# Optimization experiments

Hardware: AMD Instinct MI355X
Metric: run time of the kernel (lower is better)

The kernel has to match this reference:

```python
import jax, jax.numpy as jnp
import numpy as np
import math

B = 2; SEQ = 4096; D_MODEL = 768; D_STATE = 128; D_CONV = 4; EXPAND = 2; HEAD_DIM = 64
D_INNER = EXPAND * D_MODEL; D_SSM = D_INNER; NH = D_SSM // HEAD_DIM  # 24 heads
CONV_DIM = D_SSM + 2 * D_STATE; CHUNK = 256
D_IN_PROJ = 2 * D_INNER + 2 * D_STATE + NH


def causal_conv1d(x, w, b):
    # x: [B, C, L]; w: [C, W] depthwise kernel; left-pad for causality; silu activation
    W = w.shape[-1]; L = x.shape[-1]
    xp = jnp.pad(x, ((0, 0), (0, 0), (W - 1, 0)))
    y = b[None, :, None] + sum(xp[:, :, k:k + L] * w[None, :, k, None] for k in range(W))
    return jax.nn.silu(y)


def segsum(a):
    # a: [..., S] -> [..., S, S]; entry (i,j) = sum_{k=j+1..i} a_k for i>=j, -inf above diag
    S = a.shape[-1]
    cs = jnp.cumsum(a, -1)
    d = cs[..., :, None] - cs[..., None, :]
    mask = jnp.tril(jnp.ones((S, S), bool))
    return jnp.where(mask, d, -jnp.inf)


def ssd_chunk_scan(x, dt, A, Bm, Cm, Dp, chunk):
    # Mamba2 SSD chunked selective scan. x:[b,l,h,p] dt:[b,l,h] A:[h] Bm,Cm:[b,l,n] Dp:[h]
    b, l, h, p = x.shape; n = Bm.shape[-1]; nc = l // chunk
    xc = x.reshape(b, nc, chunk, h, p)
    Bc = Bm.reshape(b, nc, chunk, n)
    Cc = Cm.reshape(b, nc, chunk, n)
    dtc = dt.reshape(b, nc, chunk, h)
    a = jnp.transpose(A[None, None, None, :] * dtc, (0, 3, 1, 2))  # [b,h,c,s]
    Acs = jnp.cumsum(a, -1)
    Lm = jnp.exp(segsum(a))  # [b,h,c,s,s] lower-triangular decay
    # intra-chunk (diagonal block) outputs
    Ydiag = jnp.einsum('bcsn,bczn,bhcsz,bczh,bczhp->bcshp', Cc, Bc, Lm, dtc, xc)
    # per-chunk end states
    decay_states = jnp.exp(Acs[..., -1:] - Acs)  # [b,h,c,s]
    states = jnp.einsum('bczn,bhcz,bczh,bczhp->bchpn', Bc, decay_states, dtc, xc)
    # inter-chunk recurrence over nc chunks (small) via scan
    decay_chunk = jnp.exp(Acs[..., -1])  # [b,h,c]
    def step(hcar, inp):
        dcy, st = inp
        return dcy[..., None, None] * hcar + st, hcar  # emit state entering chunk
    _, prev = jax.lax.scan(step, jnp.zeros_like(states[:, 0]),
                           (jnp.moveaxis(decay_chunk, -1, 0), jnp.moveaxis(states, 1, 0)))
    prev = jnp.moveaxis(prev, 0, 1)  # [b,c,h,p,n]
    Yoff = jnp.einsum('bcsn,bchpn,bhcs->bcshp', Cc, prev, jnp.exp(Acs))
    return (Ydiag + Yoff).reshape(b, l, h, p) + Dp[None, None, :, None] * x


def _forward(u, time_diff, W_in, b_in, conv_w, conv_b, tconv1_w, tconv1_b,
             tconv2_w, tconv2_b, mlp_w1, mlp_b1, mlp_w2, mlp_b2, gate_w, gate_b,
             ln_w, ln_b, A_log, dt_bias, Dp, norm_w, W_out, b_out):
    silu = jax.nn.silu
    zxbcdt = u @ W_in.T + b_in  # [B,L,d_in_proj], d_mlp=0
    z = zxbcdt[..., :D_SSM]
    xBC = zxbcdt[..., D_SSM:D_SSM + CONV_DIM]
    dt = zxbcdt[..., D_SSM + CONV_DIM:]  # [B,L,H]
    A = -jnp.exp(A_log)
    xBC = jnp.transpose(causal_conv1d(jnp.transpose(xBC, (0, 2, 1)), conv_w, conv_b), (0, 2, 1))
    # time-gated dt path (time_diff: [B,H,L])
    ts = silu(time_diff @ mlp_w1.T + mlp_b1) @ mlp_w2.T + mlp_b2
    tdt = ts * time_diff
    tdt = causal_conv1d(tdt, tconv1_w, tconv1_b)
    tdt = causal_conv1d(tdt, tconv2_w, tconv2_b)  # [B,H,L]
    final_dt = dt * jnp.transpose(tdt, (0, 2, 1))
    x = xBC[..., :D_SSM]
    Bm = xBC[..., D_SSM:D_SSM + D_STATE]
    Cm = xBC[..., D_SSM + D_STATE:]
    dt_sp = jax.nn.softplus(final_dt + dt_bias)
    xh = x.reshape(x.shape[0], x.shape[1], NH, HEAD_DIM)
    y = ssd_chunk_scan(xh, dt_sp, A, Bm, Cm, Dp, CHUNK).reshape(x.shape[0], x.shape[1], D_SSM)
    # gated RMSNorm (norm_before_gate=False): gate first, then normalize
    yg = y * silu(z)
    y = yg * jax.lax.rsqrt(jnp.mean(yg * yg, -1, keepdims=True) + 1e-12) * norm_w
    out = y @ W_out.T + b_out
    # time residual gate + LayerNorm over seq_len
    tg = jax.nn.sigmoid(time_diff @ gate_w.T + gate_b)  # [B,H,1]
    tmix = tg * time_diff + (1.0 - tg) * tdt
    mu = jnp.mean(tmix, -1, keepdims=True)
    var = jnp.mean((tmix - mu) ** 2, -1, keepdims=True)
    time_out = (tmix - mu) * jax.lax.rsqrt(var + 1e-12) * ln_w + ln_b
    return out, time_out


def setup_inputs():
    key = jax.random.key(0)
    ks = jax.random.split(key, 16)
    def nrm(k, shape, scale=0.02):
        return jax.random.normal(k, shape, jnp.float32) * scale
    dtv = jnp.exp(jax.random.uniform(ks[10], (NH,), jnp.float32) * (math.log(0.1) - math.log(0.001)) + math.log(0.001))
    dtv = jnp.clip(dtv, 1e-4)
    dt_bias = dtv + jnp.log(-jnp.expm1(-dtv))
    A_log = jnp.log(jax.random.uniform(ks[11], (NH,), jnp.float32, 1.0, 16.0))
    return dict(
        u=jax.random.normal(ks[0], (B, SEQ, D_MODEL), jnp.float32),
        time_diff=jax.random.uniform(ks[1], (B, NH, SEQ), jnp.float32),
        W_in=nrm(ks[2], (D_IN_PROJ, D_MODEL)), b_in=jnp.zeros((D_IN_PROJ,), jnp.float32),
        conv_w=nrm(ks[3], (CONV_DIM, D_CONV), 0.2), conv_b=jnp.zeros((CONV_DIM,), jnp.float32),
        tconv1_w=nrm(ks[4], (NH, D_CONV), 0.2), tconv1_b=jnp.zeros((NH,), jnp.float32),
        tconv2_w=nrm(ks[5], (NH, D_CONV), 0.2), tconv2_b=jnp.zeros((NH,), jnp.float32),
        mlp_w1=nrm(ks[6], (SEQ, SEQ)), mlp_b1=jnp.zeros((SEQ,), jnp.float32),
        mlp_w2=nrm(ks[7], (SEQ, SEQ)), mlp_b2=jnp.zeros((SEQ,), jnp.float32),
        gate_w=nrm(ks[8], (1, SEQ)), gate_b=jnp.zeros((1,), jnp.float32),
        ln_w=jnp.ones((SEQ,), jnp.float32), ln_b=jnp.zeros((SEQ,), jnp.float32),
        A_log=A_log, dt_bias=dt_bias, Dp=jnp.ones((NH,), jnp.float32),
        norm_w=jnp.ones((D_SSM,), jnp.float32),
        W_out=nrm(ks[9], (D_MODEL, D_INNER)), b_out=jnp.zeros((D_MODEL,), jnp.float32),
    )


def reference(u, time_diff, W_in, b_in, conv_w, conv_b, tconv1_w, tconv1_b,
              tconv2_w, tconv2_b, mlp_w1, mlp_b1, mlp_w2, mlp_b2, gate_w, gate_b,
              ln_w, ln_b, A_log, dt_bias, Dp, norm_w, W_out, b_out):
    return _forward(u, time_diff, W_in, b_in, conv_w, conv_b, tconv1_w, tconv1_b,
                    tconv2_w, tconv2_b, mlp_w1, mlp_b1, mlp_w2, mlp_b2, gate_w, gate_b,
                    ln_w, ln_b, A_log, dt_bias, Dp, norm_w, W_out, b_out)
```

## Files before the change

### kernel.cpp

```cpp
#include <hip/hip_runtime.h>
#include <math.h>

#define BB 2
#define SEQ 4096
#define DMODEL 768
#define DSTATE 128
#define NHH 24
#define HDIM 64
#define DSSM 1536
#define CDIM 1792
#define CHK 256
#define NC 16
#define DPROJ 3352
#define MR (BB*SEQ)
#define KSPLIT 32
#define XSTR 1920
#define CT 16
#define SXS 270
#define STS 134

typedef __attribute__((ext_vector_type(8))) short bf16x8;
typedef __attribute__((ext_vector_type(8))) unsigned short u16x8;
typedef __attribute__((ext_vector_type(4))) float f32x4;

__device__ __forceinline__ float siluf(float x) { return x / (1.0f + expf(-x)); }

__device__ __forceinline__ unsigned short f2bf(float f) {
    unsigned u = __float_as_uint(f);
    unsigned r = (u + 0x7fffu + ((u >> 16) & 1u)) >> 16;
    return (unsigned short)r;
}

__device__ __forceinline__ float bf2f(unsigned short u) {
    return __uint_as_float(((unsigned)u) << 16);
}

__device__ __forceinline__ float4 bf2f4(ushort4 v) {
    float4 o;
    o.x = bf2f(v.x); o.y = bf2f(v.y); o.z = bf2f(v.z); o.w = bf2f(v.w);
    return o;
}

__device__ __forceinline__ void gload_lds16(const void* g, void* l) {
    __builtin_amdgcn_global_load_lds((const __attribute__((address_space(1))) unsigned int*)g,
                                     (__attribute__((address_space(3))) unsigned int*)l, 16, 0, 0);
}

__global__ __launch_bounds__(256) void cvt_bf16_k(const float* __restrict__ in,
    unsigned short* __restrict__ out, int n_valid, int n_total)
{
    int i = (blockIdx.x * 256 + threadIdx.x) * 4;
    if (i >= n_total) return;
    ushort4 o;
    if (i + 3 < n_valid) {
        float4 v = *(const float4*)&in[i];
        o.x = f2bf(v.x); o.y = f2bf(v.y); o.z = f2bf(v.z); o.w = f2bf(v.w);
    } else {
        o.x = (i + 0 < n_valid) ? f2bf(in[i + 0]) : 0;
        o.y = (i + 1 < n_valid) ? f2bf(in[i + 1]) : 0;
        o.z = (i + 2 < n_valid) ? f2bf(in[i + 2]) : 0;
        o.w = (i + 3 < n_valid) ? f2bf(in[i + 3]) : 0;
    }
    *(ushort4*)&out[i] = o;
}

__global__ __launch_bounds__(256) void gemm_mfma_dual(
    const unsigned short* __restrict__ A,
    const unsigned short* __restrict__ B1, const float* __restrict__ bias1,
    unsigned short* __restrict__ C1, int N1, int NT1, int nbias1, int NWG1,
    const unsigned short* __restrict__ B2, const float* __restrict__ bias2,
    unsigned short* __restrict__ C2, int N2, int NT2, int nbias2,
    int K, int KT)
{
    __shared__ unsigned short SMEM[24576];
    const int tid = threadIdx.x;
    const int w = tid >> 6, l = tid & 63;
    const int wr = w >> 1, wc = w & 1;
    const int lr = l & 15, lk = l >> 4;
    int nwg = gridDim.x, bid = blockIdx.x;
    int wg = (nwg & 7) ? bid : ((bid & 7) * (nwg >> 3) + (bid >> 3));
    const unsigned short* B;
    const float* bias;
    unsigned short* C;
    int N, NT, nbias;
    if (wg < NWG1) { B = B1; bias = bias1; C = C1; N = N1; NT = NT1; nbias = nbias1; }
    else { wg -= NWG1; B = B2; bias = bias2; C = C2; N = N2; NT = NT2; nbias = nbias2; }
    const int m0 = (wg / NT) * 128, n0 = (wg % NT) * 128;
    f32x4 acc[4][4] = {};
    const int i16 = w * 64 + l;
    const int row0 = i16 >> 2, sl = i16 & 3;
    const size_t ga0 = (size_t)(m0 + row0) * K + sl * 8;
    const size_t ga1 = (size_t)(m0 + row0 + 64) * K + sl * 8;
    const size_t gb0 = (size_t)(n0 + row0) * K + sl * 8;
    const size_t gb1 = (size_t)(n0 + row0 + 64) * K + sl * 8;
    const int lo0 = (w * 64) * 8;
    const int lo1 = (256 + w * 64) * 8;

#define STAGE(bb, kt) { int ko = (kt) * 32; int bs = (bb) * 8192;            \
      gload_lds16(A + ga0 + ko, &SMEM[bs + lo0]);                            \
      gload_lds16(A + ga1 + ko, &SMEM[bs + lo1]);                            \
      gload_lds16(B + gb0 + ko, &SMEM[bs + 4096 + lo0]);                     \
      gload_lds16(B + gb1 + ko, &SMEM[bs + 4096 + lo1]); }

    STAGE(0, 0);
    STAGE(1, 1);
    for (int kt = 0; kt < KT; ++kt) {
        if (kt + 1 < KT) {
            asm volatile("s_waitcnt vmcnt(4)" ::: "memory");
        } else {
            asm volatile("s_waitcnt vmcnt(0)" ::: "memory");
        }
        __builtin_amdgcn_s_barrier();
        if (kt + 2 < KT) STAGE((kt + 2) % 3, kt + 2);
        int bs = (kt % 3) * 8192;
        bf16x8 af[4], bg[4];
#pragma unroll
        for (int mi = 0; mi < 4; ++mi)
            af[mi] = *(const bf16x8*)&SMEM[bs + (wr * 64 + mi * 16 + lr) * 32 + lk * 8];
#pragma unroll
        for (int nj = 0; nj < 4; ++nj)
            bg[nj] = *(const bf16x8*)&SMEM[bs + 4096 + (wc * 64 + nj * 16 + lr) * 32 + lk * 8];
#pragma unroll
        for (int mi = 0; mi < 4; ++mi)
#pragma unroll
            for (int nj = 0; nj < 4; ++nj)
                acc[mi][nj] = __builtin_amdgcn_mfma_f32_16x16x32_bf16(af[mi], bg[nj], acc[mi][nj], 0, 0, 0);
    }
#undef STAGE
    {
        unsigned short* CL = SMEM;
#pragma unroll
        for (int half = 0; half < 2; ++half) {
            __syncthreads();
            if (wr == half) {
#pragma unroll
                for (int nj = 0; nj < 4; ++nj) {
                    int col = n0 + wc * 64 + nj * 16 + lr;
                    float bz = (col < nbias) ? bias[col] : 0.f;
                    int cl = wc * 64 + nj * 16 + lr;
#pragma unroll
                    for (int mi = 0; mi < 4; ++mi)
#pragma unroll
                        for (int r = 0; r < 4; ++r)
                            CL[(mi * 16 + lk * 4 + r) * 136 + cl] = f2bf(acc[mi][nj][r] + bz);
                }
            }
            __syncthreads();
            for (int i = tid; i < 1024; i += 256) {
                int rr = i >> 4, c8 = (i & 15) * 8;
                int m = m0 + half * 64 + rr;
                *(u16x8*)&C[(size_t)m * N + n0 + c8] = *(const u16x8*)&CL[rr * 136 + c8];
            }
        }
    }
}

__global__ __launch_bounds__(256) void gemm_skinny_nt(const float* __restrict__ A,
    const float* __restrict__ Bw, float* __restrict__ part, int N, int K)
{
    __shared__ float sA[48 * 33];
    __shared__ float sB[128 * 33];
    const int nb = blockIdx.x, kb = blockIdx.y;
    const int n0 = nb * 128;
    const int KS = K / KSPLIT;
    const int k0 = kb * KS;
    const int tid = threadIdx.x;
    const int tx = tid & 31, ty = tid >> 5;
    float acc[6][4] = {{0.f}};
    for (int kc = 0; kc < KS; kc += 32) {
        if (kc) __syncthreads();
        for (int i = tid; i < 384; i += 256) {
            int m = i >> 3, k4 = (i & 7) * 4;
            float4 v = *(const float4*)&A[(size_t)m * K + k0 + kc + k4];
            sA[m * 33 + k4 + 0] = v.x; sA[m * 33 + k4 + 1] = v.y;
            sA[m * 33 + k4 + 2] = v.z; sA[m * 33 + k4 + 3] = v.w;
        }
        for (int i = tid; i < 1024; i += 256) {
            int n = i >> 3, k4 = (i & 7) * 4;
            float4 v = *(const float4*)&Bw[(size_t)(n0 + n) * K + k0 + kc + k4];
            sB[n * 33 + k4 + 0] = v.x; sB[n * 33 + k4 + 1] = v.y;
            sB[n * 33 + k4 + 2] = v.z; sB[n * 33 + k4 + 3] = v.w;
        }
        __syncthreads();
#pragma unroll 8
        for (int kk = 0; kk < 32; ++kk) {
            float a[6], b[4];
#pragma unroll
            for (int r = 0; r < 6; ++r) a[r] = sA[(ty * 6 + r) * 33 + kk];
#pragma unroll
            for (int j = 0; j < 4; ++j) b[j] = sB[(tx + j * 32) * 33 + kk];
#pragma unroll
            for (int r = 0; r < 6; ++r)
#pragma unroll
                for (int j = 0; j < 4; ++j)
                    acc[r][j] = fmaf(a[r], b[j], acc[r][j]);
        }
    }
    float* pb = part + (size_t)kb * 48 * N;
#pragma unroll
    for (int r = 0; r < 6; ++r)
#pragma unroll
        for (int j = 0; j < 4; ++j)
            pb[(size_t)(ty * 6 + r) * N + n0 + tx + j * 32] = acc[r][j];
}

__global__ __launch_bounds__(256) void conv_skinny_k(const unsigned short* __restrict__ xbc,
    const float* __restrict__ cw, const float* __restrict__ cb,
    unsigned short* __restrict__ out,
    const float* __restrict__ skA, const float* __restrict__ skB,
    float* __restrict__ skPart, int skN, int skK, int NWGC)
{
    __shared__ __align__(16) unsigned char SMEMRAW[23232];
    int bid = blockIdx.x;
    int tid = threadIdx.x;
    if (bid >= NWGC) {
        float* sA = (float*)SMEMRAW;
        float* sB = (float*)(SMEMRAW + 48 * 33 * 4);
        int t = bid - NWGC;
        int nb = t & 31, kb = t >> 5;
        const int n0 = nb * 128;
        const int KS = skK / KSPLIT;
        const int k0 = kb * KS;
        const int tx = tid & 31, ty = tid >> 5;
        float acc[6][4] = {{0.f}};
        for (int kc = 0; kc < KS; kc += 32) {
            if (kc) __syncthreads();
            for (int i = tid; i < 384; i += 256) {
                int m = i >> 3, k4 = (i & 7) * 4;
                float4 v = *(const float4*)&skA[(size_t)m * skK + k0 + kc + k4];
                sA[m * 33 + k4 + 0] = v.x; sA[m * 33 + k4 + 1] = v.y;
                sA[m * 33 + k4 + 2] = v.z; sA[m * 33 + k4 + 3] = v.w;
            }
            for (int i = tid; i < 1024; i += 256) {
                int n = i >> 3, k4 = (i & 7) * 4;
                float4 v = *(const float4*)&skB[(size_t)(n0 + n) * skK + k0 + kc + k4];
                sB[n * 33 + k4 + 0] = v.x; sB[n * 33 + k4 + 1] = v.y;
                sB[n * 33 + k4 + 2] = v.z; sB[n * 33 + k4 + 3] = v.w;
            }
            __syncthreads();
#pragma unroll 8
            for (int kk = 0; kk < 32; ++kk) {
                float a[6], b[4];
#pragma unroll
                for (int r = 0; r < 6; ++r) a[r] = sA[(ty * 6 + r) * 33 + kk];
#pragma unroll
                for (int j = 0; j < 4; ++j) b[j] = sB[(tx + j * 32) * 33 + kk];
#pragma unroll
                for (int r = 0; r < 6; ++r)
#pragma unroll
                    for (int j = 0; j < 4; ++j)
                        acc[r][j] = fmaf(a[r], b[j], acc[r][j]);
            }
        }
        float* pb = skPart + (size_t)kb * 48 * skN;
#pragma unroll
        for (int r = 0; r < 6; ++r)
#pragma unroll
            for (int j = 0; j < 4; ++j)
                pb[(size_t)(ty * 6 + r) * skN + n0 + tx + j * 32] = acc[r][j];
        return;
    }
    int idx = bid * 256 + tid;
    int slot = idx % 448;
    int g = idx / 448;
    int c4 = slot * 4;
    int b = g / (SEQ / CT);
    int t0 = (g % (SEQ / CT)) * CT;
    size_t rb = (size_t)b * SEQ;
    float4 cw0 = *(const float4*)&cw[(c4 + 0) * 4];
    float4 cw1 = *(const float4*)&cw[(c4 + 1) * 4];
    float4 cw2 = *(const float4*)&cw[(c4 + 2) * 4];
    float4 cw3 = *(const float4*)&cw[(c4 + 3) * 4];
    float4 cbv = *(const float4*)&cb[c4];
    float4 zero = {0.f, 0.f, 0.f, 0.f};
    float4 w0, w1, w2;
    w0 = (t0 - 3 >= 0) ? bf2f4(*(const ushort4*)&xbc[(rb + t0 - 3) * XSTR + c4]) : zero;
    w1 = (t0 - 2 >= 0) ? bf2f4(*(const ushort4*)&xbc[(rb + t0 - 2) * XSTR + c4]) : zero;
    w2 = (t0 - 1 >= 0) ? bf2f4(*(const ushort4*)&xbc[(rb + t0 - 1) * XSTR + c4]) : zero;
#pragma unroll
    for (int i = 0; i < CT; ++i) {
        int t = t0 + i;
        float4 w3 = bf2f4(*(const ushort4*)&xbc[(rb + t) * XSTR + c4]);
        float a0 = cbv.x + w0.x * cw0.x + w1.x * cw0.y + w2.x * cw0.z + w3.x * cw0.w;
        float a1 = cbv.y + w0.y * cw1.x + w1.y * cw1.y + w2.y * cw1.z + w3.y * cw1.w;
        float a2 = cbv.z + w0.z * cw2.x + w1.z * cw2.y + w2.z * cw2.z + w3.z * cw2.w;
        float a3 = cbv.w + w0.w * cw3.x + w1.w * cw3.y + w2.w * cw3.z + w3.w * cw3.w;
        ushort4 o;
        o.x = f2bf(siluf(a0)); o.y = f2bf(siluf(a1));
        o.z = f2bf(siluf(a2)); o.w = f2bf(siluf(a3));
        *(ushort4*)&out[(rb + t) * CDIM + c4] = o;
        w0 = w1; w1 = w2; w2 = w3;
    }
}

__global__ __launch_bounds__(256) void reduce_part_k(const float* __restrict__ part,
    const float* __restrict__ bias, float* __restrict__ out, int N, int act)
{
    int idx = blockIdx.x * 256 + threadIdx.x;
    if (idx >= 48 * N) return;
    int n = idx % N;
    float s = bias[n];
#pragma unroll
    for (int kb = 0; kb < KSPLIT; ++kb) s += part[(size_t)kb * 48 * N + idx];
    if (act) s = siluf(s);
    out[idx] = s;
}

__global__ __launch_bounds__(256) void time_conv_k(const float* __restrict__ ts,
    const float* __restrict__ td, const float* __restrict__ w1, const float* __restrict__ b1,
    const float* __restrict__ w2, const float* __restrict__ b2, float* __restrict__ tdt)
{
    __shared__ float u0[SEQ];
    __shared__ float u1[SEQ];
    int row = blockIdx.x, h = row % NHH;
    const float* tsr = ts + (size_t)row * SEQ;
    const float* tdr = td + (size_t)row * SEQ;
    for (int i = threadIdx.x; i < SEQ; i += 256) u0[i] = tsr[i] * tdr[i];
    __syncthreads();
    float wa[4], wb[4];
#pragma unroll
    for (int k = 0; k < 4; ++k) { wa[k] = w1[h * 4 + k]; wb[k] = w2[h * 4 + k]; }
    float ba = b1[h], bbv = b2[h];
    for (int i = threadIdx.x; i < SEQ; i += 256) {
        float acc = ba;
#pragma unroll
        for (int k = 0; k < 4; ++k) { int tt = i + k - 3; if (tt >= 0) acc = fmaf(u0[tt], wa[k], acc); }
        u1[i] = siluf(acc);
    }
    __syncthreads();
    for (int i = threadIdx.x; i < SEQ; i += 256) {
        float acc = bbv;
#pragma unroll
        for (int k = 0; k < 4; ++k) { int tt = i + k - 3; if (tt >= 0) acc = fmaf(u1[tt], wb[k], acc); }
        tdt[(size_t)row * SEQ + i] = siluf(acc);
    }
}

__global__ __launch_bounds__(256) void dtsp_cum_k(const unsigned short* __restrict__ r1,
    const float* __restrict__ tdt, const float* __restrict__ dt_bias,
    const float* __restrict__ A_log, float* __restrict__ dtp, float* __restrict__ acs)
{
    __shared__ float wsum[4];
    int blk = blockIdx.x;
    int c = blk % NC;
    int bh = blk / NC;
    int h = bh % NHH, b = bh / NHH;
    int tid = threadIdx.x;
    int s = c * CHK + tid;
    size_t base = (size_t)bh * SEQ + s;
    float x = bf2f(r1[((size_t)(b * SEQ + s)) * XSTR + CDIM + h]) * tdt[base] + dt_bias[h];
    float dt = (x > 20.0f) ? x : log1pf(expf(x));
    dtp[base] = dt;
    float Ah = -expf(A_log[h]);
    float v = Ah * dt;
    int ln = tid & 63;
#pragma unroll
    for (int off = 1; off < 64; off <<= 1) {
        float t = __shfl_up(v, off, 64);
        if (ln >= off) v += t;
    }
    if (ln == 63) wsum[tid >> 6] = v;
    __syncthreads();
    float add = 0.f;
    int wv = tid >> 6;
#pragma unroll
    for (int i = 0; i < 3; ++i)
        if (i < wv) add += wsum[i];
    acs[base] = v + add;
}

__global__ __launch_bounds__(256) void ssd_states_sraw_k(const unsigned short* __restrict__ xc,
    const float* __restrict__ dtp, const float* __restrict__ acs_g,
    float* __restrict__ st, unsigned short* __restrict__ sraw)
{
    __shared__ float s_coef[256];
    __shared__ unsigned short SXT[64 * STS];
    __shared__ unsigned short SBT[128 * STS];
    int bid = blockIdx.x;
    int blk = (gridDim.x & 7) ? bid : ((bid & 7) * (gridDim.x >> 3) + (bid >> 3));
    int tid = threadIdx.x;
    int w = tid >> 6, l = tid & 63;
    int lr = l & 15, lk = l >> 4;
    if (blk >= BB * NC * NHH) {
        int t = blk - BB * NC * NHH;
        int bc = t / 10, tile = t % 10;
        int rem = tile, st_i = 0;
        for (st_i = 0; ; ++st_i) { if (rem < st_i + 1) break; rem -= st_i + 1; }
        int zt = rem;
        int b = bc / NC, c = bc % NC;
        size_t rowbase = (size_t)b * SEQ + c * CHK;
        for (int i = tid; i < 64 * 32; i += 256) {
            int r = i >> 5, c4 = (i & 31) * 4;
            *(ushort4*)&SXT[r * STS + c4] = *(const ushort4*)&xc[(rowbase + st_i * 64 + r) * CDIM + DSSM + DSTATE + c4];
            *(ushort4*)&SBT[r * STS + c4] = *(const ushort4*)&xc[(rowbase + zt * 64 + r) * CDIM + DSSM + c4];
        }
        __syncthreads();
        f32x4 d[4] = {};
#pragma unroll
        for (int kt = 0; kt < 4; ++kt) {
            bf16x8 av = *(const bf16x8*)&SXT[(w * 16 + lr) * STS + kt * 32 + lk * 8];
            bf16x8 bv[4];
#pragma unroll
            for (int nj = 0; nj < 4; ++nj)
                bv[nj] = *(const bf16x8*)&SBT[(nj * 16 + lr) * STS + kt * 32 + lk * 8];
#pragma unroll
            for (int nj = 0; nj < 4; ++nj)
                d[nj] = __builtin_amdgcn_mfma_f32_16x16x32_bf16(av, bv[nj], d[nj], 0, 0, 0);
        }
        unsigned short* tp = sraw + (size_t)bc * 16 * 4096 + (size_t)(st_i * 4 + zt) * 4096;
#pragma unroll
        for (int nj = 0; nj < 4; ++nj)
#pragma unroll
            for (int r = 0; r < 4; ++r)
                tp[(w * 16 + lk * 4 + r) * 64 + nj * 16 + lr] = f2bf(d[nj][r]);
        return;
    }
    int h = blk % NHH, c = (blk / NHH) % NC, b = blk / (NHH * NC);
    size_t rowbase = (size_t)b * SEQ + c * CHK;
    size_t dbase = (size_t)(b * NHH + h) * SEQ + c * CHK;
    float alv = acs_g[dbase + 255];
    s_coef[tid] = expf(alv - acs_g[dbase + tid]) * dtp[dbase + tid];
    __syncthreads();
    f32x4 acc[4][2] = {};
    for (int z0 = 0; z0 < CHK; z0 += 128) {
        if (z0) __syncthreads();
        for (int i = tid; i < 128 * 8; i += 256) {
            int zz = i >> 3, p8 = (i & 7) * 8;
            float sc = s_coef[z0 + zz];
            u16x8 v = *(const u16x8*)&xc[(rowbase + z0 + zz) * CDIM + h * HDIM + p8];
#pragma unroll
            for (int e = 0; e < 8; ++e)
                SXT[(p8 + e) * STS + zz] = f2bf(bf2f(v[e]) * sc);
        }
        for (int i = tid; i < 128 * 16; i += 256) {
            int zz = i >> 4, n8 = (i & 15) * 8;
            u16x8 v = *(const u16x8*)&xc[(rowbase + z0 + zz) * CDIM + DSSM + n8];
#pragma unroll
            for (int e = 0; e < 8; ++e)
                SBT[(n8 + e) * STS + zz] = v[e];
        }
        __syncthreads();
#pragma unroll
        for (int kt = 0; kt < 4; ++kt) {
            bf16x8 av[4], bv[2];
#pragma unroll
            for (int mi = 0; mi < 4; ++mi)
                av[mi] = *(const bf16x8*)&SXT[(mi * 16 + lr) * STS + kt * 32 + lk * 8];
#pragma unroll
            for (int nj = 0; nj < 2; ++nj)
                bv[nj] = *(const bf16x8*)&SBT[(w * 32 + nj * 16 + lr) * STS + kt * 32 + lk * 8];
#pragma unroll
            for (int mi = 0; mi < 4; ++mi)
#pragma unroll
                for (int nj = 0; nj < 2; ++nj)
                    acc[mi][nj] = __builtin_amdgcn_mfma_f32_16x16x32_bf16(av[mi], bv[nj], acc[mi][nj], 0, 0, 0);
        }
    }
    size_t base = (size_t)blk * (HDIM * DSTATE);
#pragma unroll
    for (int mi = 0; mi < 4; ++mi)
#pragma unroll
        for (int r = 0; r < 4; ++r) {
            int p = mi * 16 + lk * 4 + r;
#pragma unroll
            for (int nj = 0; nj < 2; ++nj)
                st[base + p * DSTATE + w * 32 + nj * 16 + lr] = acc[mi][nj][r];
        }
}

__global__ __launch_bounds__(256) void ssd_scan_k(const float* __restrict__ st,
    const float* __restrict__ acs_g, unsigned short* __restrict__ pv16)
{
    int b = blockIdx.x / NHH, h = blockIdx.x % NHH;
    int tid = threadIdx.x;
    float carry[32];
#pragma unroll
    for (int j = 0; j < 32; ++j) carry[j] = 0.f;
    for (int c = 0; c < NC; ++c) {
        int bch = (b * NC + c) * NHH + h;
        size_t base = (size_t)bch * (HDIM * DSTATE);
        float dcy = expf(acs_g[(size_t)(b * NHH + h) * SEQ + c * CHK + 255]);
#pragma unroll
        for (int j = 0; j < 32; ++j) {
            pv16[base + tid + j * 256] = f2bf(carry[j]);
            carry[j] = fmaf(dcy, carry[j], st[base + tid + j * 256]);
        }
    }
}

__global__ __launch_bounds__(256) void ssd_y2_k(const unsigned short* __restrict__ xc,
    const float* __restrict__ dtp, const float* __restrict__ acs_g,
    const unsigned short* __restrict__ sraw, const unsigned short* __restrict__ pv16,
    const float* __restrict__ Dp, unsigned short* __restrict__ Ybf)
{
    __shared__ unsigned short SXT[32 * SXS];
    int bid = blockIdx.x;
    int blk2 = (gridDim.x & 7) ? bid : ((bid & 7) * (gridDim.x >> 3) + (bid >> 3));
    int half = blk2 & 1;
    int blk = blk2 >> 1;
    int h = blk % NHH;
    int c = (blk / NHH) % NC;
    int b = blk / (NHH * NC);
    int tid = threadIdx.x;
    int w = tid >> 6, l = tid & 63;
    int lr = l & 15, lk = l >> 4;
    int pbase = half * 32;
    size_t rowbase = (size_t)b * SEQ + c * CHK;
    size_t dbase = (size_t)(b * NHH + h) * SEQ + c * CHK;
    for (int i = tid; i < 256 * 4; i += 256) {
        int z = i >> 2, p8 = (i & 3) * 8;
        float az0q = acs_g[dbase + (z & 192)];
        float e = az0q - acs_g[dbase + z];
        if (e > 60.f) e = 60.f;
        float sc = expf(e) * dtp[dbase + z];
        u16x8 v = *(const u16x8*)&xc[(rowbase + z) * CDIM + h * HDIM + pbase + p8];
#pragma unroll
        for (int e2 = 0; e2 < 8; ++e2)
            SXT[(p8 + e2) * SXS + z] = f2bf(bf2f(v[e2]) * sc);
    }
    float az0w = acs_g[dbase + w * 64];
    float esw[4][4];
#pragma unroll
    for (int mi = 0; mi < 4; ++mi)
#pragma unroll
        for (int r = 0; r < 4; ++r)
            esw[mi][r] = expf(acs_g[dbase + w * 64 + mi * 16 + lk * 4 + r] - az0w);
    __syncthreads();

    const unsigned short* tbase = sraw + (size_t)(b * NC + c) * 16 * 4096;
    const unsigned short* pvbase = pv16 + (size_t)blk * (HDIM * DSTATE);
    f32x4 acc[4][2] = {};
    for (int zt = 0; zt < w; ++zt) {
        const unsigned short* tp = tbase + (size_t)(w * 4 + zt) * 4096;
        f32x4 tmp[4][2] = {};
#pragma unroll
        for (int kt = 0; kt < 2; ++kt) {
            bf16x8 av[4], bv[2];
#pragma unroll
            for (int mi = 0; mi < 4; ++mi)
                av[mi] = *(const bf16x8*)&tp[(mi * 16 + lr) * 64 + kt * 32 + lk * 8];
#pragma unroll
            for (int nj = 0; nj < 2; ++nj)
                bv[nj] = *(const bf16x8*)&SXT[(nj * 16 + lr) * SXS + zt * 64 + kt * 32 + lk * 8];
#pragma unroll
            for (int mi = 0; mi < 4; ++mi)
#pragma unroll
                for (int nj = 0; nj < 2; ++nj)
                    tmp[mi][nj] = __builtin_amdgcn_mfma_f32_16x16x32_bf16(av[mi], bv[nj], tmp[mi][nj], 0, 0, 0);
        }
        float rho = expf(az0w - acs_g[dbase + zt * 64]);
#pragma unroll
        for (int mi = 0; mi < 4; ++mi)
#pragma unroll
            for (int r = 0; r < 4; ++r) {
                float es = esw[mi][r] * rho;
#pragma unroll
                for (int nj = 0; nj < 2; ++nj)
                    acc[mi][nj][r] += es * tmp[mi][nj][r];
            }
    }
    {
        const unsigned short* tp = tbase + (size_t)(w * 4 + w) * 4096;
        f32x4 tmp[4][2] = {};
#pragma unroll
        for (int kt = 0; kt < 2; ++kt) {
            bf16x8 av[4], bv[2];
#pragma unroll
            for (int mi = 0; mi < 4; ++mi) {
                av[mi] = *(const bf16x8*)&tp[(mi * 16 + lr) * 64 + kt * 32 + lk * 8];
                int zb = kt * 32 + lk * 8;
                int sl = mi * 16 + lr;
#pragma unroll
                for (int e = 0; e < 8; ++e)
                    if (zb + e > sl) av[mi][e] = 0;
            }
#pragma unroll
            for (int nj = 0; nj < 2; ++nj)
                bv[nj] = *(const bf16x8*)&SXT[(nj * 16 + lr) * SXS + w * 64 + kt * 32 + lk * 8];
#pragma unroll
            for (int mi = 0; mi < 4; ++mi)
#pragma unroll
                for (int nj = 0; nj < 2; ++nj)
                    tmp[mi][nj] = __builtin_amdgcn_mfma_f32_16x16x32_bf16(av[mi], bv[nj], tmp[mi][nj], 0, 0, 0);
        }
#pragma unroll
        for (int mi = 0; mi < 4; ++mi)
#pragma unroll
            for (int r = 0; r < 4; ++r) {
                float es = esw[mi][r];
#pragma unroll
                for (int nj = 0; nj < 2; ++nj)
                    acc[mi][nj][r] += es * tmp[mi][nj][r];
            }
    }
    {
        f32x4 tmp[4][2] = {};
#pragma unroll
        for (int kt = 0; kt < 4; ++kt) {
            bf16x8 av[4], bv[2];
#pragma unroll
            for (int mi = 0; mi < 4; ++mi)
                av[mi] = *(const bf16x8*)&xc[(rowbase + w * 64 + mi * 16 + lr) * CDIM + DSSM + DSTATE + kt * 32 + lk * 8];
#pragma unroll
            for (int nj = 0; nj < 2; ++nj)
                bv[nj] = *(const bf16x8*)&pvbase[(pbase + nj * 16 + lr) * DSTATE + kt * 32 + lk * 8];
#pragma unroll
            for (int mi = 0; mi < 4; ++mi)
#pragma unroll
                for (int nj = 0; nj < 2; ++nj)
                    tmp[mi][nj] = __builtin_amdgcn_mfma_f32_16x16x32_bf16(av[mi], bv[nj], tmp[mi][nj], 0, 0, 0);
        }
        float eoff = expf(az0w);
#pragma unroll
        for (int mi = 0; mi < 4; ++mi)
#pragma unroll
            for (int r = 0; r < 4; ++r) {
                float es = esw[mi][r] * eoff;
#pragma unroll
                for (int nj = 0; nj < 2; ++nj)
                    acc[mi][nj][r] += es * tmp[mi][nj][r];
            }
    }
    float dph = Dp[h];
#pragma unroll
    for (int mi = 0; mi < 4; ++mi) {
#pragma unroll
        for (int r = 0; r < 4; ++r) {
            int s = w * 64 + mi * 16 + lk * 4 + r;
#pragma unroll
            for (int nj = 0; nj < 2; ++nj) {
                int p = pbase + nj * 16 + lr;
                float xv = bf2f(xc[(rowbase + s) * CDIM + h * HDIM + p]);
                Ybf[(rowbase + s) * DSSM + h * HDIM + p] = f2bf(acc[mi][nj][r] + dph * xv);
            }
        }
    }
}

__global__ __launch_bounds__(256) void rmsnorm_k(const unsigned short* __restrict__ Ybf_in,
    const unsigned short* __restrict__ zbf, const float* __restrict__ nw,
    unsigned short* __restrict__ Ybf_out)
{
    __shared__ float red[8];
    int row = blockIdx.x;
    const unsigned short* y = Ybf_in + (size_t)row * DSSM;
    const unsigned short* z = zbf + (size_t)row * DSSM;
    float v[6];
    float ss = 0.f;
#pragma unroll
    for (int k = 0; k < 6; ++k) {
        int i = threadIdx.x + k * 256;
        float g = bf2f(y[i]) * siluf(bf2f(z[i]));
        v[k] = g;
        ss = fmaf(g, g, ss);
    }
#pragma unroll
    for (int o = 32; o > 0; o >>= 1) ss += __shfl_down(ss, o, 64);
    int wv = threadIdx.x >> 6, ln = threadIdx.x & 63;
    if (ln == 0) red[wv] = ss;
    __syncthreads();
    float tot = red[0] + red[1] + red[2] + red[3];
    float sc = rsqrtf(tot / (float)DSSM + 1e-12f);
    unsigned short* yo = Ybf_out + (size_t)row * DSSM;
#pragma unroll
    for (int k = 0; k < 6; ++k) {
        int i = threadIdx.x + k * 256;
        yo[i] = f2bf(v[k] * sc * nw[i]);
    }
}

__global__ __launch_bounds__(256) void gemm_out_timeout_k(
    const unsigned short* __restrict__ A, const unsigned short* __restrict__ B,
    const float* __restrict__ bias, float* __restrict__ C, int N, int K, int KT, int NT, int NWGG,
    const float* __restrict__ td, const float* __restrict__ tdt,
    const float* __restrict__ gw, const float* __restrict__ gb,
    const float* __restrict__ lnw, const float* __restrict__ lnb, float* __restrict__ out2)
{
    __shared__ __align__(16) unsigned char SMEMRAW[49152];
    unsigned short* SMEM = (unsigned short*)SMEMRAW;
    const int tid = threadIdx.x;
    int nwg = gridDim.x, bid = blockIdx.x;
    int wg = (nwg & 7) ? bid : ((bid & 7) * (nwg >> 3) + (bid >> 3));
    if (wg >= NWGG) {
        float* tm = (float*)SMEMRAW;
        __shared__ float red[8];
        int row = wg - NWGG;
        const float* tdr = td + (size_t)row * SEQ;
        const float* tdtr = tdt + (size_t)row * SEQ;
        int wv = tid >> 6, ln = tid & 63;
        float part = 0.f;
        for (int i = tid; i < SEQ; i += 256) part = fmaf(tdr[i], gw[i], part);
#pragma unroll
        for (int o = 32; o > 0; o >>= 1) part += __shfl_down(part, o, 64);
        if (ln == 0) red[wv] = part;
        __syncthreads();
        float dot = red[0] + red[1] + red[2] + red[3];
        float tg = 1.f / (1.f + expf(-(dot + gb[0])));
        __syncthreads();
        float sum = 0.f;
        for (int i = tid; i < SEQ; i += 256) {
            float x = tg * tdr[i] + (1.f - tg) * tdtr[i];
            tm[i] = x;
            sum += x;
        }
#pragma unroll
        for (int o = 32; o > 0; o >>= 1) sum += __shfl_down(sum, o, 64);
        if (ln == 0) red[wv] = sum;
        __syncthreads();
        float mu = (red[0] + red[1] + red[2] + red[3]) / (float)SEQ;
        __syncthreads();
        float s2 = 0.f;
        for (int i = tid; i < SEQ; i += 256) { float d = tm[i] - mu; s2 = fmaf(d, d, s2); }
#pragma unroll
        for (int o = 32; o > 0; o >>= 1) s2 += __shfl_down(s2, o, 64);
        if (ln == 0) red[wv] = s2;
        __syncthreads();
        float var = (red[0] + red[1] + red[2] + red[3]) / (float)SEQ;
        float inv = rsqrtf(var + 1e-12f);
        for (int i = tid; i < SEQ; i += 256)
            out2[(size_t)row * SEQ + i] = (tm[i] - mu) * inv * lnw[i] + lnb[i];
        return;
    }
    const int w = tid >> 6, l = tid & 63;
    const int wr = w >> 1, wc = w & 1;
    const int lr = l & 15, lk = l >> 4;
    const int m0 = (wg / NT) * 128, n0 = (wg % NT) * 128;
    f32x4 acc[4][4] = {};
    const int i16 = w * 64 + l;
    const int row0 = i16 >> 2, sl = i16 & 3;
    const size_t ga0 = (size_t)(m0 + row0) * K + sl * 8;
    const size_t ga1 = (size_t)(m0 + row0 + 64) * K + sl * 8;
    const size_t gb0 = (size_t)(n0 + row0) * K + sl * 8;
    const size_t gb1 = (size_t)(n0 + row0 + 64) * K + sl * 8;
    const int lo0 = (w * 64) * 8;
    const int lo1 = (256 + w * 64) * 8;

#define STAGE3(bb, kt) { int ko = (kt) * 32; int bs = (bb) * 8192;           \
      gload_lds16(A + ga0 + ko, &SMEM[bs + lo0]);                            \
      gload_lds16(A + ga1 + ko, &SMEM[bs + lo1]);                            \
      gload_lds16(B + gb0 + ko, &SMEM[bs + 4096 + lo0]);                     \
      gload_lds16(B + gb1 + ko, &SMEM[bs + 4096 + lo1]); }

    STAGE3(0, 0);
    STAGE3(1, 1);
    for (int kt = 0; kt < KT; ++kt) {
        if (kt + 1 < KT) {
            asm volatile("s_waitcnt vmcnt(4)" ::: "memory");
        } else {
            asm volatile("s_waitcnt vmcnt(0)" ::: "memory");
        }
        __builtin_amdgcn_s_barrier();
        if (kt + 2 < KT) STAGE3((kt + 2) % 3, kt + 2);
        int bs = (kt % 3) * 8192;
        bf16x8 af[4], bg[4];
#pragma unroll
        for (int mi = 0; mi < 4; ++mi)
            af[mi] = *(const bf16x8*)&SMEM[bs + (wr * 64 + mi * 16 + lr) * 32 + lk * 8];
#pragma unroll
        for (int nj = 0; nj < 4; ++nj)
            bg[nj] = *(const bf16x8*)&SMEM[bs + 4096 + (wc * 64 + nj * 16 + lr) * 32 + lk * 8];
#pragma unroll
        for (int mi = 0; mi < 4; ++mi)
#pragma unroll
            for (int nj = 0; nj < 4; ++nj)
                acc[mi][nj] = __builtin_amdgcn_mfma_f32_16x16x32_bf16(af[mi], bg[nj], acc[mi][nj], 0, 0, 0);
    }
#undef STAGE3
#pragma unroll
    for (int nj = 0; nj < 4; ++nj) {
        int col = n0 + wc * 64 + nj * 16 + lr;
        float bz = bias[col];
#pragma unroll
        for (int mi = 0; mi < 4; ++mi) {
#pragma unroll
            for (int r = 0; r < 4; ++r) {
                int m = m0 + wr * 64 + mi * 16 + lk * 4 + r;
                C[(size_t)m * N + col] = acc[mi][nj][r] + bz;
            }
        }
    }
}

extern "C" void kernel_launch(void* const* d_in, const int* in_sizes, int n_in,
                              void* d_out, int out_size, void* d_ws, size_t ws_size,
                              hipStream_t stream)
{
    const float* u      = (const float*)d_in[0];
    const float* td     = (const float*)d_in[1];
    const float* W_in   = (const float*)d_in[2];
    const float* b_in   = (const float*)d_in[3];
    const float* conv_w = (const float*)d_in[4];
    const float* conv_b = (const float*)d_in[5];
    const float* t1w    = (const float*)d_in[6];
    const float* t1b    = (const float*)d_in[7];
    const float* t2w    = (const float*)d_in[8];
    const float* t2b    = (const float*)d_in[9];
    const float* m1w    = (const float*)d_in[10];
    const float* m1b    = (const float*)d_in[11];
    const float* m2w    = (const float*)d_in[12];
    const float* m2b    = (const float*)d_in[13];
    const float* gw     = (const float*)d_in[14];
    const float* gb     = (const float*)d_in[15];
    const float* lnw    = (const float*)d_in[16];
    const float* lnb    = (const float*)d_in[17];
    const float* A_log  = (const float*)d_in[18];
    const float* dt_bias= (const float*)d_in[19];
    const float* Dpv    = (const float*)d_in[20];
    const float* nw     = (const float*)d_in[21];
    const float* W_out  = (const float*)d_in[22];
    const float* b_out  = (const float*)d_in[23];
    float* out  = (float*)d_out;
    float* out2 = out + (size_t)MR * DMODEL;

    float* ws = (float*)d_ws;
    size_t o = 0;
    float* zbuf  = ws + o; o += (size_t)MR * DSSM;
    float* r1    = ws + o; o += (size_t)MR * DSSM;
    float* xcv   = ws + o; o += (size_t)MR * CDIM / 2;
    float* partb = ws + o; o += (size_t)KSPLIT * 48 * SEQ;
    float* hid   = ws + o; o += (size_t)BB * NHH * SEQ;
    float* tss   = ws + o; o += (size_t)BB * NHH * SEQ;
    float* tdt   = ws + o; o += (size_t)BB * NHH * SEQ;
    float* dtp   = ws + o; o += (size_t)MR * NHH;
    float* acs_g = ws + o; o += (size_t)MR * NHH;
    float* pvb   = ws + o; o += (size_t)BB * NC * NHH * HDIM * DSTATE;
    unsigned short* sraw = (unsigned short*)(ws + o); o += (size_t)BB * NC * 16 * 4096 / 2;
    unsigned short* r1b = (unsigned short*)r1;
    float* stb = r1;
    unsigned short* ybf16 = (unsigned short*)r1;
    unsigned short* xcv_bf = (unsigned short*)xcv;
    unsigned short* u_bf  = (unsigned short*)pvb;
    unsigned short* Wi_bf = (unsigned short*)(pvb + 3145728);
    unsigned short* pv16  = (unsigned short*)pvb;
    unsigned short* zbf   = (unsigned short*)zbuf;
    unsigned short* Y_bf  = (unsigned short*)xcv;
    unsigned short* Wo_bf = (unsigned short*)(zbuf + 6291456);

    dim3 blk(256);
    const int NWG1 = (XSTR / 128) * (MR / 128);
    const int NWGSK = (SEQ / 128) * KSPLIT;
    const int NWGC = 448 * (MR / CT) / 256;

    cvt_bf16_k<<<dim3((MR * DMODEL / 4 + 255) / 256), blk, 0, stream>>>(u, u_bf, MR * DMODEL, MR * DMODEL);
    cvt_bf16_k<<<dim3((3456 * DMODEL / 4 + 255) / 256), blk, 0, stream>>>(W_in, Wi_bf, DPROJ * DMODEL, 3456 * DMODEL);
    cvt_bf16_k<<<dim3((DMODEL * DSSM / 4 + 255) / 256), blk, 0, stream>>>(W_out, Wo_bf, DMODEL * DSSM, DMODEL * DSSM);
    gemm_skinny_nt<<<dim3(SEQ / 128, KSPLIT), blk, 0, stream>>>(td, m1w, partb, SEQ, SEQ);
    gemm_mfma_dual<<<dim3(NWG1 + (DSSM / 128) * (MR / 128)), blk, 0, stream>>>(
        u_bf,
        Wi_bf + (size_t)DSSM * DMODEL, b_in + DSSM, r1b, XSTR, XSTR / 128, DPROJ - DSSM, NWG1,
        Wi_bf, b_in, zbf, DSSM, DSSM / 128, DSSM,
        DMODEL, DMODEL / 32);
    reduce_part_k<<<dim3((48 * SEQ + 255) / 256), blk, 0, stream>>>(partb, m1b, hid, SEQ, 1);
    conv_skinny_k<<<dim3(NWGC + NWGSK), blk, 0, stream>>>(
        r1b, conv_w, conv_b, xcv_bf, hid, m2w, partb, SEQ, SEQ, NWGC);
    reduce_part_k<<<dim3((48 * SEQ + 255) / 256), blk, 0, stream>>>(partb, m2b, tss, SEQ, 0);
    time_conv_k<<<dim3(BB * NHH), blk, 0, stream>>>(tss, td, t1w, t1b, t2w, t2b, tdt);
    dtsp_cum_k<<<dim3(BB * NHH * NC), blk, 0, stream>>>(r1b, tdt, dt_bias, A_log, dtp, acs_g);
    ssd_states_sraw_k<<<dim3(BB * NC * NHH + BB * NC * 10), blk, 0, stream>>>(xcv_bf, dtp, acs_g, stb, sraw);
    ssd_scan_k<<<dim3(BB * NHH), blk, 0, stream>>>(stb, acs_g, pv16);
    ssd_y2_k<<<dim3(BB * NC * NHH * 2), blk, 0, stream>>>(xcv_bf, dtp, acs_g, sraw, pv16, Dpv, ybf16);
    rmsnorm_k<<<dim3(MR), blk, 0, stream>>>(ybf16, zbf, nw, Y_bf);
    gemm_out_timeout_k<<<dim3((DMODEL / 128) * (MR / 128) + BB * NHH), blk, 0, stream>>>(
        Y_bf, Wo_bf, b_out, out, DMODEL, DSSM, DSSM / 32, DMODEL / 128, (DMODEL / 128) * (MR / 128),
        td, tdt, gw, gb, lnw, lnb, out2);
}
```

Baseline: 353.2 us.

## Use bf16 MFMA for skinny time-MLP GEMMs and unfuse conv launch

Replaces the fp32 LDS-tiled FMA skinny GEMM (48x4096 by 4096x4096, split-K) with a version that loads fp32 rows directly from global memory, packs them to bf16 in registers and runs 16x16x32 bf16 MFMA without shared memory. The second MLP GEMM is no longer fused into the conv kernel's grid; it gets its own launch followed by a standalone conv kernel. This is meant to cut the ALU cost of the large fp32 weight GEMMs. It costs bf16 rounding of the weights and activations, and one extra kernel launch.

Measured after the change: 329.2 us. -6.8%, faster.

```diff
diff --git a/kernel.cpp b/kernel.cpp
--- a/kernel.cpp
+++ b/kernel.cpp
@@ -39,6 +39,13 @@
     float4 o;
     o.x = bf2f(v.x); o.y = bf2f(v.y); o.z = bf2f(v.z); o.w = bf2f(v.w);
     return o;
+}
+
+__device__ __forceinline__ bf16x8 pack8(float4 a, float4 b) {
+    u16x8 r;
+    r[0] = f2bf(a.x); r[1] = f2bf(a.y); r[2] = f2bf(a.z); r[3] = f2bf(a.w);
+    r[4] = f2bf(b.x); r[5] = f2bf(b.y); r[6] = f2bf(b.z); r[7] = f2bf(b.w);
+    return *(bf16x8*)&r;
 }
 
 __device__ __forceinline__ void gload_lds16(const void* g, void* l) {
@@ -155,112 +162,53 @@
     }
 }
 
-__global__ __launch_bounds__(256) void gemm_skinny_nt(const float* __restrict__ A,
+__global__ __launch_bounds__(256) void gemm_skinny_mfma(const float* __restrict__ A,
     const float* __restrict__ Bw, float* __restrict__ part, int N, int K)
 {
-    __shared__ float sA[48 * 33];
-    __shared__ float sB[128 * 33];
     const int nb = blockIdx.x, kb = blockIdx.y;
     const int n0 = nb * 128;
     const int KS = K / KSPLIT;
     const int k0 = kb * KS;
     const int tid = threadIdx.x;
-    const int tx = tid & 31, ty = tid >> 5;
-    float acc[6][4] = {{0.f}};
-    for (int kc = 0; kc < KS; kc += 32) {
-        if (kc) __syncthreads();
-        for (int i = tid; i < 384; i += 256) {
-            int m = i >> 3, k4 = (i & 7) * 4;
-            float4 v = *(const float4*)&A[(size_t)m * K + k0 + kc + k4];
-            sA[m * 33 + k4 + 0] = v.x; sA[m * 33 + k4 + 1] = v.y;
-            sA[m * 33 + k4 + 2] = v.z; sA[m * 33 + k4 + 3] = v.w;
-        }
-        for (int i = tid; i < 1024; i += 256) {
-            int n = i >> 3, k4 = (i & 7) * 4;
-            float4 v = *(const float4*)&Bw[(size_t)(n0 + n) * K + k0 + kc + k4];
-            sB[n * 33 + k4 + 0] = v.x; sB[n * 33 + k4 + 1] = v.y;
-            sB[n * 33 + k4 + 2] = v.z; sB[n * 33 + k4 + 3] = v.w;
-        }
-        __syncthreads();
-#pragma unroll 8
-        for (int kk = 0; kk < 32; ++kk) {
-            float a[6], b[4];
-#pragma unroll
-            for (int r = 0; r < 6; ++r) a[r] = sA[(ty * 6 + r) * 33 + kk];
-#pragma unroll
-            for (int j = 0; j < 4; ++j) b[j] = sB[(tx + j * 32) * 33 + kk];
-#pragma unroll
-            for (int r = 0; r < 6; ++r)
-#pragma unroll
-                for (int j = 0; j < 4; ++j)
-                    acc[r][j] = fmaf(a[r], b[j], acc[r][j]);
-        }
+    const int w = tid >> 6, l = tid & 63;
+    const int lr = l & 15, lk = l >> 4;
+    const int nw0 = n0 + w * 32;
+    f32x4 acc[3][2] = {};
+    for (int kt = 0; kt < KS; kt += 32) {
+        int kk = k0 + kt + lk * 8;
+        bf16x8 af[3], bfr[2];
+#pragma unroll
+        for (int mi = 0; mi < 3; ++mi) {
+            const float* ap = &A[(size_t)(mi * 16 + lr) * K + kk];
+            af[mi] = pack8(*(const float4*)ap, *(const float4*)(ap + 4));
+        }
+#pragma unroll
+        for (int nf = 0; nf < 2; ++nf) {
+            const float* bp = &Bw[(size_t)(nw0 + nf * 16 + lr) * K + kk];
+            bfr[nf] = pack8(*(const float4*)bp, *(const float4*)(bp + 4));
+        }
+#pragma unroll
+        for (int mi = 0; mi < 3; ++mi)
+#pragma unroll
+            for (int nf = 0; nf < 2; ++nf)
+                acc[mi][nf] = __builtin_amdgcn_mfma_f32_16x16x32_bf16(af[mi], bfr[nf], acc[mi][nf], 0, 0, 0);
     }
     float* pb = part + (size_t)kb * 48 * N;
 #pragma unroll
-    for (int r = 0; r < 6; ++r)
-#pragma unroll
-        for (int j = 0; j < 4; ++j)
-            pb[(size_t)(ty * 6 + r) * N + n0 + tx + j * 32] = acc[r][j];
-}
-
-__global__ __launch_bounds__(256) void conv_skinny_k(const unsigned short* __restrict__ xbc,
+    for (int mi = 0; mi < 3; ++mi)
+#pragma unroll
+        for (int r = 0; r < 4; ++r)
+#pragma unroll
+            for (int nf = 0; nf < 2; ++nf)
+                pb[(size_t)(mi * 16 + lk * 4 + r) * N + nw0 + nf * 16 + lr] = acc[mi][nf][r];
+}
+
+__global__ __launch_bounds__(256) void conv_xbc_k(const unsigned short* __restrict__ xbc,
     const float* __restrict__ cw, const float* __restrict__ cb,
-    unsigned short* __restrict__ out,
-    const float* __restrict__ skA, const float* __restrict__ skB,
-    float* __restrict__ skPart, int skN, int skK, int NWGC)
-{
-    __shared__ __align__(16) unsigned char SMEMRAW[23232];
-    int bid = blockIdx.x;
-    int tid = threadIdx.x;
-    if (bid >= NWGC) {
-        float* sA = (float*)SMEMRAW;
-        float* sB = (float*)(SMEMRAW + 48 * 33 * 4);
-        int t = bid - NWGC;
-        int nb = t & 31, kb = t >> 5;
-        const int n0 = nb * 128;
-        const int KS = skK / KSPLIT;
-        const int k0 = kb * KS;
-        const int tx = tid & 31, ty = tid >> 5;
-        float acc[6][4] = {{0.f}};
-        for (int kc = 0; kc < KS; kc += 32) {
-            if (kc) __syncthreads();
-            for (int i = tid; i < 384; i += 256) {
-                int m = i >> 3, k4 = (i & 7) * 4;
-                float4 v = *(const float4*)&skA[(size_t)m * skK + k0 + kc + k4];
-                sA[m * 33 + k4 + 0] = v.x; sA[m * 33 + k4 + 1] = v.y;
-                sA[m * 33 + k4 + 2] = v.z; sA[m * 33 + k4 + 3] = v.w;
-            }
-            for (int i = tid; i < 1024; i += 256) {
-                int n = i >> 3, k4 = (i & 7) * 4;
-                float4 v = *(const float4*)&skB[(size_t)(n0 + n) * skK + k0 + kc + k4];
-                sB[n * 33 + k4 + 0] = v.x; sB[n * 33 + k4 + 1] = v.y;
-                sB[n * 33 + k4 + 2] = v.z; sB[n * 33 + k4 + 3] = v.w;
-            }
-            __syncthreads();
-#pragma unroll 8
-            for (int kk = 0; kk < 32; ++kk) {
-                float a[6], b[4];
-#pragma unroll
-                for (int r = 0; r < 6; ++r) a[r] = sA[(ty * 6 + r) * 33 + kk];
-#pragma unroll
-                for (int j = 0; j < 4; ++j) b[j] = sB[(tx + j * 32) * 33 + kk];
-#pragma unroll
-                for (int r = 0; r < 6; ++r)
-#pragma unroll
-                    for (int j = 0; j < 4; ++j)
-                        acc[r][j] = fmaf(a[r], b[j], acc[r][j]);
-            }
-        }
-        float* pb = skPart + (size_t)kb * 48 * skN;
-#pragma unroll
-        for (int r = 0; r < 6; ++r)
-#pragma unroll
-            for (int j = 0; j < 4; ++j)
-                pb[(size_t)(ty * 6 + r) * skN + n0 + tx + j * 32] = acc[r][j];
-        return;
-    }
-    int idx = bid * 256 + tid;
+    unsigned short* __restrict__ out)
+{
+    int idx = blockIdx.x * 256 + threadIdx.x;
+    if (idx >= 448 * (MR / CT)) return;
     int slot = idx % 448;
     int g = idx / 448;
     int c4 = slot * 4;
@@ -838,21 +786,19 @@
 
     dim3 blk(256);
     const int NWG1 = (XSTR / 128) * (MR / 128);
-    const int NWGSK = (SEQ / 128) * KSPLIT;
-    const int NWGC = 448 * (MR / CT) / 256;
 
     cvt_bf16_k<<<dim3((MR * DMODEL / 4 + 255) / 256), blk, 0, stream>>>(u, u_bf, MR * DMODEL, MR * DMODEL);
     cvt_bf16_k<<<dim3((3456 * DMODEL / 4 + 255) / 256), blk, 0, stream>>>(W_in, Wi_bf, DPROJ * DMODEL, 3456 * DMODEL);
     cvt_bf16_k<<<dim3((DMODEL * DSSM / 4 + 255) / 256), blk, 0, stream>>>(W_out, Wo_bf, DMODEL * DSSM, DMODEL * DSSM);
-    gemm_skinny_nt<<<dim3(SEQ / 128, KSPLIT), blk, 0, stream>>>(td, m1w, partb, SEQ, SEQ);
+    gemm_skinny_mfma<<<dim3(SEQ / 128, KSPLIT), blk, 0, stream>>>(td, m1w, partb, SEQ, SEQ);
     gemm_mfma_dual<<<dim3(NWG1 + (DSSM / 128) * (MR / 128)), blk, 0, stream>>>(
         u_bf,
         Wi_bf + (size_t)DSSM * DMODEL, b_in + DSSM, r1b, XSTR, XSTR / 128, DPROJ - DSSM, NWG1,
         Wi_bf, b_in, zbf, DSSM, DSSM / 128, DSSM,
         DMODEL, DMODEL / 32);
     reduce_part_k<<<dim3((48 * SEQ + 255) / 256), blk, 0, stream>>>(partb, m1b, hid, SEQ, 1);
-    conv_skinny_k<<<dim3(NWGC + NWGSK), blk, 0, stream>>>(
-        r1b, conv_w, conv_b, xcv_bf, hid, m2w, partb, SEQ, SEQ, NWGC);
+    gemm_skinny_mfma<<<dim3(SEQ / 128, KSPLIT), blk, 0, stream>>>(hid, m2w, partb, SEQ, SEQ);
+    conv_xbc_k<<<dim3((448 * (MR / CT) + 255) / 256), blk, 0, stream>>>(r1b, conv_w, conv_b, xcv_bf);
     reduce_part_k<<<dim3((48 * SEQ + 255) / 256), blk, 0, stream>>>(partb, m2b, tss, SEQ, 0);
     time_conv_k<<<dim3(BB * NHH), blk, 0, stream>>>(tss, td, t1w, t1b, t2w, t2b, tdt);
     dtsp_cum_k<<<dim3(BB * NHH * NC), blk, 0, stream>>>(r1b, tdt, dt_bias, A_log, dtp, acs_g);
```
